# Performance work log

Measured on AMD Instinct MI355X. Metric: run time of the kernel, lower is better.

Reference implementation:

```python
import math
import jax, jax.numpy as jnp
import numpy as np

B, L, D_MODEL = 2, 2048, 768
H = 12            # num_heads == num_key_value_heads
FEAT = 16         # feature_dim
HEAD_DIM = D_MODEL // H  # 64


def taylor_exp(x):
    """Taylor-exp feature map: phi(x) = [1, x/rrd, (x (x) x)/(sqrt(2)*rd)].
    x: [..., d] -> [..., 1 + d + d^2]"""
    d = x.shape[-1]
    rd = math.sqrt(d)
    rrd = math.sqrt(rd)
    r2 = math.sqrt(2.0)
    x2 = (x[..., :, None] * x[..., None, :]).reshape(*x.shape[:-1], d * d) / r2
    ones = jnp.ones(x.shape[:-1] + (1,), dtype=x.dtype)
    return jnp.concatenate([ones, x / rrd, x2 / rd], axis=-1)


def setup_inputs() -> dict:
    key = jax.random.key(0)
    k1, k2, k3, k4, k5 = jax.random.split(key, 5)
    s = 0.02
    return {
        "hidden_states": jax.random.normal(k1, (B, L, D_MODEL), jnp.float32),
        "Wq": jax.random.normal(k2, (H * FEAT, D_MODEL), jnp.float32) * s,
        "Wk": jax.random.normal(k3, (H * FEAT, D_MODEL), jnp.float32) * s,
        "Wv": jax.random.normal(k4, (D_MODEL, D_MODEL), jnp.float32) * s,
        "Wo": jax.random.normal(k5, (D_MODEL, D_MODEL), jnp.float32) * s,
    }


def reference(hidden_states, Wq, Wk, Wv, Wo):
    b, l, d = hidden_states.shape
    # projections (torch Linear, no bias): y = x @ W.T
    q = jnp.einsum('bld,fd->blf', hidden_states, Wq).reshape(b, l, H, FEAT).transpose(0, 2, 1, 3)
    k = jnp.einsum('bld,fd->blf', hidden_states, Wk).reshape(b, l, H, FEAT).transpose(0, 2, 1, 3)
    v = jnp.einsum('bld,fd->blf', hidden_states, Wv).reshape(b, l, H, HEAD_DIM).transpose(0, 2, 1, 3)

    q = taylor_exp(q)   # [b,h,l,Dexp]
    k = taylor_exp(k)   # k_enc == k (forward clones k), v_enc == v

    # denominator: k_enc.sum over seq + causal cumsum of k
    k_state = jnp.sum(k, axis=2, keepdims=True) + jnp.cumsum(k, axis=2)  # [b,h,l,Dexp]
    z = 1.0 / jnp.sum(q * k_state, axis=-1)                              # [b,h,l]

    # quadratic scores; y1 uses causal (tril) mask, y2 uses full scores with same k,v
    A = jnp.einsum('bhnd,bhmd->bhnm', q, k)                              # [b,h,l,l]
    causal = jnp.tril(jnp.ones((l, l), dtype=A.dtype))
    A_total = A * causal + A                                             # tril(A) + A
    y = jnp.einsum('bhnm,bhme->bhne', A_total, v) * z[..., None]         # [b,h,l,e]

    out = y.transpose(0, 2, 1, 3).reshape(b, l, H * HEAD_DIM)
    return jnp.einsum('blf,df->bld', out, Wo)
```

## Files before the change

### kernel.cpp

```cpp
#include <hip/hip_runtime.h>

typedef unsigned short ushortT;
typedef __bf16 bf16x8 __attribute__((ext_vector_type(8)));
typedef float f32x4 __attribute__((ext_vector_type(4)));

#define BB   2
#define LL   2048
#define DM   768
#define HH   12
#define FT   16
#define HD   64
#define DEXP 273
#define CH   128
#define NC   16
#define NBH  24
#define NBLK 384
#define C2f  0.17677669529663687f
#define KH   768
#define KP   1536
#define SLAB_US   4096
#define SPK_BLK_US 36864
#define SPK_BLK_B  73728

__device__ __forceinline__ void split_bf16(float x, ushortT& hi, ushortT& lo) {
  unsigned b = __float_as_uint(x);
  unsigned r = b + 0x7FFFu + ((b >> 16) & 1u);
  hi = (ushortT)(r >> 16);
  float hf = __uint_as_float((unsigned)hi << 16);
  lo = (ushortT)(__float_as_uint(x - hf) >> 16);
}

__global__ __launch_bounds__(256) void pack_a(const float* __restrict__ X,
                                              ushortT* __restrict__ Xh,
                                              int total4) {
  int g = blockIdx.x * 256 + threadIdx.x;
  if (g >= total4) return;
  int m = g / 192, k4 = (g % 192) * 4;
  float4 v = *(const float4*)(X + (size_t)m * 768 + k4);
  ushortT h[4], l[4];
  split_bf16(v.x, h[0], l[0]);
  split_bf16(v.y, h[1], l[1]);
  split_bf16(v.z, h[2], l[2]);
  split_bf16(v.w, h[3], l[3]);
  ushortT* p = Xh + (size_t)m * KP + k4;
  *(ushort4*)p = *(ushort4*)h;
  *(ushort4*)(p + KH) = *(ushort4*)l;
}

__global__ __launch_bounds__(256) void pack_w(const float* __restrict__ W0,
                                              const float* __restrict__ W1,
                                              const float* __restrict__ W2,
                                              int n1, int n2,
                                              ushortT* __restrict__ Wh,
                                              int total4) {
  int g = blockIdx.x * 256 + threadIdx.x;
  if (g >= total4) return;
  int n = g / 192, k4 = (g % 192) * 4;
  const float* src = (n < n1 ? W0 + (size_t)n * 768
                    : n < n2 ? W1 + (size_t)(n - n1) * 768
                             : W2 + (size_t)(n - n2) * 768);
  float4 v = *(const float4*)(src + k4);
  ushortT h[4], l[4];
  split_bf16(v.x, h[0], l[0]);
  split_bf16(v.y, h[1], l[1]);
  split_bf16(v.z, h[2], l[2]);
  split_bf16(v.w, h[3], l[3]);
  ushortT* p = Wh + (size_t)n * KP + k4;
  *(ushort4*)p = *(ushort4*)h;
  *(ushort4*)(p + KH) = *(ushort4*)l;
}

typedef const __attribute__((address_space(1))) unsigned gq_t;
typedef __attribute__((address_space(3))) unsigned lq_t;
__device__ __forceinline__ void gload_lds16(const ushortT* g, ushortT* l) {
  __builtin_amdgcn_global_load_lds((gq_t*)g, (lq_t*)l, 16, 0, 0);
}

__global__ __launch_bounds__(512, 4) void mfma_gemm(const ushortT* __restrict__ A,
                                                    const ushortT* __restrict__ B,
                                                    float* __restrict__ Y, int ldy,
                                                    int ntiles) {
  __shared__ ushortT sAh[2][128 * 32], sAl[2][128 * 32];
  __shared__ ushortT sBh[2][64 * 32], sBl[2][64 * 32];
  const int blk = blockIdx.x;
  const int xcd = blk & 7, slot = blk >> 3;
  const int mtp = gridDim.x / (8 * ntiles);
  const int mt = xcd * mtp + slot / ntiles;
  const int nt = slot % ntiles;
  const int bm = mt * 128, bn = nt * 64;
  const int tid = threadIdx.x, wave = tid >> 6, lane = tid & 63;
  const int srow = lane >> 2, schk = (lane & 3) * 8;
  const ushortT* gsrc;
  ushortT* lb0;
  ushortT* lb1;
  int iters;
  switch (wave) {
    case 0:  gsrc = A + (size_t)(bm + srow) * KP + schk;           lb0 = sAh[0];        lb1 = sAh[1];        iters = 4; break;
    case 1:  gsrc = A + (size_t)(bm + 64 + srow) * KP + schk;      lb0 = sAh[0] + 2048; lb1 = sAh[1] + 2048; iters = 4; break;
    case 2:  gsrc = A + (size_t)(bm + srow) * KP + KH + schk;      lb0 = sAl[0];        lb1 = sAl[1];        iters = 4; break;
    case 3:  gsrc = A + (size_t)(bm + 64 + srow) * KP + KH + schk; lb0 = sAl[0] + 2048; lb1 = sAl[1] + 2048; iters = 4; break;
    case 4:  gsrc = B + (size_t)(bn + srow) * KP + schk;           lb0 = sBh[0];        lb1 = sBh[1];        iters = 2; break;
    case 5:  gsrc = B + (size_t)(bn + 32 + srow) * KP + schk;      lb0 = sBh[0] + 1024; lb1 = sBh[1] + 1024; iters = 2; break;
    case 6:  gsrc = B + (size_t)(bn + srow) * KP + KH + schk;      lb0 = sBl[0];        lb1 = sBl[1];        iters = 2; break;
    default: gsrc = B + (size_t)(bn + 32 + srow) * KP + KH + schk; lb0 = sBl[0] + 1024; lb1 = sBl[1] + 1024; iters = 2; break;
  }
  const int wm = (wave >> 1) * 32, wn = (wave & 1) * 32;
  const int fr = lane & 15, quad = lane >> 4;
  f32x4 acc[2][2] = {};
  for (int it = 0; it < iters; it++)
    gload_lds16(gsrc + (size_t)it * 16 * KP, lb0 + it * 512);
  __syncthreads();
#pragma unroll 2
  for (int step = 0; step < 24; step++) {
    const int cur = step & 1;
    if (step < 23) {
      ushortT* lbn = cur ? lb0 : lb1;
      const int k1 = (step + 1) * 32;
      for (int it = 0; it < iters; it++)
        gload_lds16(gsrc + k1 + (size_t)it * 16 * KP, lbn + it * 512);
    }
    const ushortT* pAh = sAh[cur];
    const ushortT* pAl = sAl[cur];
    const ushortT* pBh = sBh[cur];
    const ushortT* pBl = sBl[cur];
    bf16x8 ah[2], al[2], bh2[2], bl2[2];
#pragma unroll
    for (int mi = 0; mi < 2; mi++) {
      ah[mi] = *(const bf16x8*)&pAh[(wm + mi * 16 + fr) * 32 + quad * 8];
      al[mi] = *(const bf16x8*)&pAl[(wm + mi * 16 + fr) * 32 + quad * 8];
    }
#pragma unroll
    for (int ni = 0; ni < 2; ni++) {
      bh2[ni] = *(const bf16x8*)&pBh[(wn + ni * 16 + fr) * 32 + quad * 8];
      bl2[ni] = *(const bf16x8*)&pBl[(wn + ni * 16 + fr) * 32 + quad * 8];
    }
#pragma unroll
    for (int mi = 0; mi < 2; mi++)
#pragma unroll
      for (int ni = 0; ni < 2; ni++) {
        acc[mi][ni] = __builtin_amdgcn_mfma_f32_16x16x32_bf16(ah[mi], bh2[ni], acc[mi][ni], 0, 0, 0);
        acc[mi][ni] = __builtin_amdgcn_mfma_f32_16x16x32_bf16(ah[mi], bl2[ni], acc[mi][ni], 0, 0, 0);
        acc[mi][ni] = __builtin_amdgcn_mfma_f32_16x16x32_bf16(al[mi], bh2[ni], acc[mi][ni], 0, 0, 0);
      }
    __syncthreads();
  }
  const int orow = quad * 4;
#pragma unroll
  for (int mi = 0; mi < 2; mi++)
#pragma unroll
    for (int ni = 0; ni < 2; ni++) {
      float* yp = Y + (size_t)(bm + wm + mi * 16 + orow) * ldy + bn + wn + ni * 16 + fr;
#pragma unroll
      for (int r = 0; r < 4; r++) yp[(size_t)r * ldy] = acc[mi][ni][r];
    }
}

__global__ __launch_bounds__(512, 4) void chunk_sum_kernel(
    const float* __restrict__ qkv, ushortT* __restrict__ Spk,
    float* __restrict__ csk) {
  const int blk = blockIdx.x;
  const int bh = blk >> 4, c = blk & 15;
  const int b = bh / HH, h = bh % HH;
  __shared__ float kT[16][128];
  __shared__ ushortT phiA[288][72];
  __shared__ ushortT Vt[64][72];
  const float* base = qkv + (size_t)(b * LL + c * CH) * 1152;
  const int tid = threadIdx.x;
  const int wave = tid >> 6, lane = tid & 63;
  const int fr = lane & 15, quad = lane >> 4;
  {
    const int m = tid >> 2, i4 = (tid & 3) * 4;
    float4 k4 = *(const float4*)&base[(size_t)m * 1152 + 192 + h * 16 + i4];
    kT[i4 + 0][m] = k4.x; kT[i4 + 1][m] = k4.y;
    kT[i4 + 2][m] = k4.z; kT[i4 + 3][m] = k4.w;
  }
  const int wm2 = (wave & 1) * 144;
  const int wn2 = (wave >> 1) * 16;
  f32x4 acc[9] = {};
  __syncthreads();
#pragma unroll 1
  for (int s = 0; s < 4; s++) {
    const int m0 = s * 32;
    if (s) __syncthreads();
    {
      const int m = m0 + (tid >> 4), e4 = (tid & 15) * 4;
      float4 v4 = *(const float4*)&base[(size_t)m * 1152 + 384 + h * 64 + e4];
      ushortT hh[4], ll[4];
      split_bf16(v4.x, hh[0], ll[0]); split_bf16(v4.y, hh[1], ll[1]);
      split_bf16(v4.z, hh[2], ll[2]); split_bf16(v4.w, hh[3], ll[3]);
      const int mi2 = m - m0;
#pragma unroll
      for (int j = 0; j < 4; j++) {
        Vt[e4 + j][mi2] = hh[j];
        Vt[e4 + j][32 + mi2] = ll[j];
      }
    }
    for (int idx = tid; idx < 576; idx += 512) {
      const int f = idx >> 1, hf = (idx & 1) * 16;
      const float* pa = (f >= 17) ? kT[(f - 17) >> 4] : (f >= 1 ? kT[f - 1] : kT[0]);
      const float* pb = (f >= 17) ? kT[(f - 17) & 15] : kT[0];
      const float sc = (f == 0) ? 1.0f : (f < 17 ? 0.5f : C2f);
      const bool quadf = (f >= 17);
      const bool valid = (f < DEXP);
      ushortT hrow[16], lrow[16];
#pragma unroll
      for (int g = 0; g < 4; g++) {
        float4 a4 = *(const float4*)&pa[m0 + hf + g * 4];
        float4 b4 = *(const float4*)&pb[m0 + hf + g * 4];
        float v0, v1, v2, v3;
        if (f == 0) {
          v0 = v1 = v2 = v3 = 1.0f;
        } else if (!quadf) {
          v0 = sc * a4.x; v1 = sc * a4.y; v2 = sc * a4.z; v3 = sc * a4.w;
        } else {
          v0 = sc * a4.x * b4.x; v1 = sc * a4.y * b4.y;
          v2 = sc * a4.z * b4.z; v3 = sc * a4.w * b4.w;
        }
        if (!valid) { v0 = v1 = v2 = v3 = 0.0f; }
        split_bf16(v0, hrow[g * 4 + 0], lrow[g * 4 + 0]);
        split_bf16(v1, hrow[g * 4 + 1], lrow[g * 4 + 1]);
        split_bf16(v2, hrow[g * 4 + 2], lrow[g * 4 + 2]);
        split_bf16(v3, hrow[g * 4 + 3], lrow[g * 4 + 3]);
      }
      *(uint4*)&phiA[f][hf] = *(uint4*)&hrow[0];
      *(uint4*)&phiA[f][hf + 8] = *(uint4*)&hrow[8];
      *(uint4*)&phiA[f][32 + hf] = *(uint4*)&lrow[0];
      *(uint4*)&phiA[f][32 + hf + 8] = *(uint4*)&lrow[8];
    }
    __syncthreads();
    bf16x8 bhf = *(const bf16x8*)&Vt[wn2 + fr][quad * 8];
    bf16x8 blf = *(const bf16x8*)&Vt[wn2 + fr][32 + quad * 8];
#pragma unroll
    for (int mi = 0; mi < 9; mi++) {
      bf16x8 ah = *(const bf16x8*)&phiA[wm2 + mi * 16 + fr][quad * 8];
      bf16x8 al = *(const bf16x8*)&phiA[wm2 + mi * 16 + fr][32 + quad * 8];
      acc[mi] = __builtin_amdgcn_mfma_f32_16x16x32_bf16(ah, bhf, acc[mi], 0, 0, 0);
      acc[mi] = __builtin_amdgcn_mfma_f32_16x16x32_bf16(ah, blf, acc[mi], 0, 0, 0);
      acc[mi] = __builtin_amdgcn_mfma_f32_16x16x32_bf16(al, bhf, acc[mi], 0, 0, 0);
    }
  }
  for (int f = tid; f < DEXP; f += 512) {
    float sum = 0.0f;
    if (f == 0) {
      sum = (float)CH;
    } else if (f < 17) {
      const float* p = kT[f - 1];
      for (int m = 0; m < CH; m += 4) {
        float4 x = *(const float4*)&p[m];
        sum += x.x + x.y + x.z + x.w;
      }
      sum *= 0.5f;
    } else {
      const float* pa2 = kT[(f - 17) >> 4];
      const float* pb2 = kT[(f - 17) & 15];
      for (int m = 0; m < CH; m += 4) {
        float4 x = *(const float4*)&pa2[m];
        float4 y = *(const float4*)&pb2[m];
        sum += x.x * y.x + x.y * y.y + x.z * y.z + x.w * y.w;
      }
      sum *= C2f;
    }
    csk[(size_t)blk * DEXP + f] = sum;
  }
  __syncthreads();
  ushortT* stage = &phiA[0][0];
  ushortT* Sp = Spk + (size_t)blk * SPK_BLK_US;
#pragma unroll 1
  for (int sl = 0; sl < 9; sl++) {
    if (sl) __syncthreads();
#pragma unroll
    for (int mi = 0; mi < 9; mi++) {
      const int fb = wm2 + mi * 16;
      if ((fb >> 5) == sl) {
        const int fi0 = (fb & 31) + quad * 4;
        const int gh = fi0 >> 3;
        const int inner = (fi0 << 1) & 15;
        const int e = wn2 + fr;
        const int es = (e & 7) << 4;
        ushortT hh2[4], ll2[4];
#pragma unroll
        for (int r = 0; r < 4; r++) split_bf16(acc[mi][r], hh2[r], ll2[r]);
        char* rowp = (char*)stage + e * 128;
        *(ushort4*)(rowp + ((gh << 4) ^ es) + inner) = *(ushort4*)hh2;
        *(ushort4*)(rowp + (((gh + 4) << 4) ^ es) + inner) = *(ushort4*)ll2;
      }
    }
    __syncthreads();
    uint4* gdst = (uint4*)(Sp + (size_t)sl * SLAB_US);
    const uint4* lsrc = (const uint4*)stage;
    gdst[tid] = lsrc[tid];
  }
}

__global__ __launch_bounds__(256) void prefix_kernel(ushortT* __restrict__ Spk,
                                                     float* __restrict__ csk) {
  const int gid = blockIdx.x * 256 + threadIdx.x;
  const int totS = NBH * 4608;
  if (gid < totS) {
    const int bh = gid / 4608;
    const int rem = gid % 4608;
    const int slab = rem >> 9;
    const int e = (rem >> 3) & 63;
    const int wp = rem & 7;
    const int es = (e & 7) << 4;
    const unsigned off_h = e * 128 + ((((wp >> 1)) << 4) ^ es) + ((wp & 1) << 3);
    const unsigned off_l = e * 128 + ((((wp >> 1) + 4) << 4) ^ es) + ((wp & 1) << 3);
    char* base = (char*)Spk + (size_t)bh * NC * SPK_BLK_B + slab * 8192;
    float r0[NC], r1[NC], r2[NC], r3[NC];
    float t0 = 0.f, t1 = 0.f, t2 = 0.f, t3 = 0.f;
#pragma unroll
    for (int cc = 0; cc < NC; cc++) {
      const char* p = base + (size_t)cc * SPK_BLK_B;
      ushort4 hw = *(const ushort4*)(p + off_h);
      ushort4 lw = *(const ushort4*)(p + off_l);
      r0[cc] = __uint_as_float((unsigned)hw.x << 16) + __uint_as_float((unsigned)lw.x << 16);
      r1[cc] = __uint_as_float((unsigned)hw.y << 16) + __uint_as_float((unsigned)lw.y << 16);
      r2[cc] = __uint_as_float((unsigned)hw.z << 16) + __uint_as_float((unsigned)lw.z << 16);
      r3[cc] = __uint_as_float((unsigned)hw.w << 16) + __uint_as_float((unsigned)lw.w << 16);
      t0 += r0[cc]; t1 += r1[cc]; t2 += r2[cc]; t3 += r3[cc];
    }
    float u0 = 0.f, u1 = 0.f, u2 = 0.f, u3 = 0.f;
#pragma unroll
    for (int cc = 0; cc < NC; cc++) {
      ushort4 hw, lw;
      split_bf16(u0 + t0, hw.x, lw.x);
      split_bf16(u1 + t1, hw.y, lw.y);
      split_bf16(u2 + t2, hw.z, lw.z);
      split_bf16(u3 + t3, hw.w, lw.w);
      char* p = base + (size_t)cc * SPK_BLK_B;
      *(ushort4*)(p + off_h) = hw;
      *(ushort4*)(p + off_l) = lw;
      u0 += r0[cc]; u1 += r1[cc]; u2 += r2[cc]; u3 += r3[cc];
    }
  } else {
    const int g2 = gid - totS;
    if (g2 < NBH * DEXP) {
      const int bh = g2 / DEXP;
      const int f = g2 % DEXP;
      float r[NC];
      float tot = 0.0f;
#pragma unroll
      for (int cc = 0; cc < NC; cc++) {
        r[cc] = csk[(size_t)(bh * NC + cc) * DEXP + f];
        tot += r[cc];
      }
      float run = 0.0f;
#pragma unroll
      for (int cc = 0; cc < NC; cc++) {
        csk[(size_t)(bh * NC + cc) * DEXP + f] = run + tot;
        run += r[cc];
      }
    }
  }
}

__global__ __launch_bounds__(512, 4) void fused_out(
    const float* __restrict__ qkv, const ushortT* __restrict__ Spk,
    const float* __restrict__ csk, ushortT* __restrict__ Ahat) {
  const int blk = blockIdx.x;
  const int bh = blk >> 4, c = blk & 15;
  const int b = bh / HH, h = bh % HH;
  __shared__ ushortT phiA[128][72];
  __shared__ ushortT GtD[2][4096];
  __shared__ ushortT qA1[128][24];
  __shared__ ushortT qA2[128][24];
  __shared__ ushortT kB[32][40];
  __shared__ ushortT gkS[9][64];
  __shared__ ushortT zero64[64];
  __shared__ ushortT onesRow[64];
  __shared__ float zl[128];
  const int tid = threadIdx.x;
  const int wv = tid >> 6, lane = tid & 63;
  const int fr = lane & 15, quad = lane >> 4;
  const int prow = tid >> 2, pq = tid & 3;
  const float* base = qkv + (size_t)(b * LL + c * CH) * 1152;
  const float* qrow = base + (size_t)prow * 1152 + h * 16;
  const ushortT* Gp = Spk + (size_t)blk * SPK_BLK_US;
  float qr[16];
#pragma unroll
  for (int i = 0; i < 4; i++) {
    float4 v = *(const float4*)(qrow + i * 4);
    qr[i * 4 + 0] = v.x; qr[i * 4 + 1] = v.y;
    qr[i * 4 + 2] = v.z; qr[i * 4 + 3] = v.w;
  }
  gload_lds16(Gp + wv * 512 + lane * 8, &GtD[0][wv * 512]);
  {
    ushortT qh4[4], ql4[4];
#pragma unroll
    for (int i = 0; i < 4; i++) split_bf16(qr[pq * 4 + i], qh4[i], ql4[i]);
    *(ushort4*)&qA1[prow][pq * 4] = *(ushort4*)qh4;
    *(ushort4*)&qA2[prow][pq * 4] = *(ushort4*)ql4;
  }
  {
    const float* gkp = csk + (size_t)blk * DEXP;
    for (int f = tid; f < 288; f += 512) {
      float v = (f < DEXP) ? gkp[f] : 0.0f;
      ushortT hh, ll;
      split_bf16(v, hh, ll);
      gkS[f >> 5][f & 31] = hh;
      gkS[f >> 5][32 + (f & 31)] = ll;
    }
  }
  if (tid < 64) {
    zero64[tid] = 0;
    onesRow[tid] = (tid < 32) ? (ushortT)0x3F80 : (ushortT)0;
  }
  f32x4 acc[5] = {};
#pragma unroll 1
  for (int s = 0; s < 9; s++) {
    __syncthreads();
    if (s < 8)
      gload_lds16(Gp + (s + 1) * SLAB_US + wv * 512 + lane * 8,
                  &GtD[(s + 1) & 1][wv * 512]);
    const int f0 = s * 32;
    {
      ushortT h8[8], l8[8];
#pragma unroll
      for (int j = 0; j < 8; j++) {
        const int f = f0 + pq * 8 + j;
        float v;
        if (f == 0) v = 1.0f;
        else if (f < 17) v = 0.5f * qr[f - 1];
        else if (f < DEXP) {
          const int ii = f - 17;
          v = C2f * qr[ii >> 4] * qr[ii & 15];
        } else v = 0.0f;
        split_bf16(v, h8[j], l8[j]);
      }
      *(uint4*)&phiA[prow][pq * 8] = *(uint4*)&h8[0];
      *(uint4*)&phiA[prow][32 + pq * 8] = *(uint4*)&l8[0];
    }
    bf16x8 ah = *(const bf16x8*)&phiA[wv * 16 + fr][quad * 8];
    bf16x8 al = *(const bf16x8*)&phiA[wv * 16 + fr][32 + quad * 8];
    const char* gt = (const char*)&GtD[s & 1][0];
    const int sw = (fr & 7) << 4;
#pragma unroll
    for (int ni = 0; ni < 4; ni++) {
      const int rb = (ni * 16 + fr) * 128;
      bf16x8 bh2 = *(const bf16x8*)(gt + rb + ((quad * 16) ^ sw));
      bf16x8 bl2 = *(const bf16x8*)(gt + rb + ((64 + quad * 16) ^ sw));
      acc[ni] = __builtin_amdgcn_mfma_f32_16x16x32_bf16(ah, bh2, acc[ni], 0, 0, 0);
      acc[ni] = __builtin_amdgcn_mfma_f32_16x16x32_bf16(ah, bl2, acc[ni], 0, 0, 0);
      acc[ni] = __builtin_amdgcn_mfma_f32_16x16x32_bf16(al, bh2, acc[ni], 0, 0, 0);
    }
    {
      const ushortT* gp = (fr == 0) ? &gkS[s][0] : &zero64[0];
      bf16x8 gh = *(const bf16x8*)(gp + quad * 8);
      bf16x8 gl = *(const bf16x8*)(gp + 32 + quad * 8);
      acc[4] = __builtin_amdgcn_mfma_f32_16x16x32_bf16(ah, gh, acc[4], 0, 0, 0);
      acc[4] = __builtin_amdgcn_mfma_f32_16x16x32_bf16(ah, gl, acc[4], 0, 0, 0);
      acc[4] = __builtin_amdgcn_mfma_f32_16x16x32_bf16(al, gh, acc[4], 0, 0, 0);
    }
  }
  __syncthreads();
  ushortT* VtF = &GtD[0][0];
#pragma unroll 1
  for (int s = 0; s < 4; s++) {
    const int m0 = s * 32;
    if (tid < 128) {
      int mL = tid >> 2, i4 = (tid & 3) * 4;
      float4 k4 = *(const float4*)&base[(size_t)(m0 + mL) * 1152 + 192 + h * 16 + i4];
      ushortT hh[4], ll[4];
      split_bf16(k4.x, hh[0], ll[0]); split_bf16(k4.y, hh[1], ll[1]);
      split_bf16(k4.z, hh[2], ll[2]); split_bf16(k4.w, hh[3], ll[3]);
      *(ushort4*)&kB[mL][i4] = *(ushort4*)hh;
      *(ushort4*)&kB[mL][16 + i4] = *(ushort4*)ll;
    }
    {
      int mL = tid >> 4, e4 = (tid & 15) * 4;
      float4 v4 = *(const float4*)&base[(size_t)(m0 + mL) * 1152 + 384 + h * 64 + e4];
      ushortT hh[4], ll[4];
      split_bf16(v4.x, hh[0], ll[0]); split_bf16(v4.y, hh[1], ll[1]);
      split_bf16(v4.z, hh[2], ll[2]); split_bf16(v4.w, hh[3], ll[3]);
#pragma unroll
      for (int j = 0; j < 4; j++) {
        VtF[(e4 + j) * 72 + mL] = hh[j];
        VtF[(e4 + j) * 72 + 32 + mL] = ll[j];
      }
    }
    __syncthreads();
    if (s <= (wv >> 1)) {
      bf16x8 a1 = *(const bf16x8*)&qA1[wv * 16 + fr][(quad & 1) * 8];
      bf16x8 a2 = *(const bf16x8*)&qA2[wv * 16 + fr][(quad & 1) * 8];
#pragma unroll
      for (int mtt = 0; mtt < 2; mtt++) {
        bf16x8 bk = *(const bf16x8*)&kB[mtt * 16 + fr][quad * 8];
        f32x4 sf = {};
        sf = __builtin_amdgcn_mfma_f32_16x16x32_bf16(a1, bk, sf, 0, 0, 0);
        sf = __builtin_amdgcn_mfma_f32_16x16x32_bf16(a2, bk, sf, 0, 0, 0);
        const int mg = m0 + mtt * 16 + fr;
#pragma unroll
        for (int r = 0; r < 4; r++) {
          const int rowL = wv * 16 + quad * 4 + r;
          const float sv = sf[r];
          const float p = (mg <= rowL) ? fmaf(sv, fmaf(sv, 0.03125f, 0.25f), 1.0f) : 0.0f;
          ushortT ph, pl;
          split_bf16(p, ph, pl);
          phiA[rowL][mtt * 16 + fr] = ph;
          phiA[rowL][32 + mtt * 16 + fr] = pl;
        }
      }
      bf16x8 ah = *(const bf16x8*)&phiA[wv * 16 + fr][quad * 8];
      bf16x8 al = *(const bf16x8*)&phiA[wv * 16 + fr][32 + quad * 8];
#pragma unroll
      for (int ni = 0; ni < 4; ni++) {
        bf16x8 bh2 = *(const bf16x8*)&VtF[(ni * 16 + fr) * 72 + quad * 8];
        bf16x8 bl2 = *(const bf16x8*)&VtF[(ni * 16 + fr) * 72 + 32 + quad * 8];
        acc[ni] = __builtin_amdgcn_mfma_f32_16x16x32_bf16(ah, bh2, acc[ni], 0, 0, 0);
        acc[ni] = __builtin_amdgcn_mfma_f32_16x16x32_bf16(ah, bl2, acc[ni], 0, 0, 0);
        acc[ni] = __builtin_amdgcn_mfma_f32_16x16x32_bf16(al, bh2, acc[ni], 0, 0, 0);
      }
      {
        const ushortT* op = (fr == 0) ? &onesRow[0] : &zero64[0];
        bf16x8 oh = *(const bf16x8*)(op + quad * 8);
        acc[4] = __builtin_amdgcn_mfma_f32_16x16x32_bf16(ah, oh, acc[4], 0, 0, 0);
        acc[4] = __builtin_amdgcn_mfma_f32_16x16x32_bf16(al, oh, acc[4], 0, 0, 0);
      }
    }
    __syncthreads();
  }
  if (fr == 0) {
#pragma unroll
    for (int r = 0; r < 4; r++) {
      const int rowL = wv * 16 + quad * 4 + r;
      zl[rowL] = 1.0f / acc[4][r];
    }
  }
  const size_t rowbase = (size_t)(b * LL + c * CH);
#pragma unroll
  for (int ni = 0; ni < 4; ni++)
#pragma unroll
    for (int r = 0; r < 4; r++) {
      const int rowL = wv * 16 + quad * 4 + r;
      const float val = acc[ni][r] * zl[rowL];
      ushortT hh, ll;
      split_bf16(val, hh, ll);
      ushortT* ap = Ahat + (rowbase + rowL) * (size_t)KP + h * 64 + ni * 16 + fr;
      ap[0] = hh;
      ap[KH] = ll;
    }
}

extern "C" void kernel_launch(void* const* d_in, const int* in_sizes, int n_in,
                              void* d_out, int out_size, void* d_ws, size_t ws_size,
                              hipStream_t stream) {
  const float* hs = (const float*)d_in[0];
  const float* Wq = (const float*)d_in[1];
  const float* Wk = (const float*)d_in[2];
  const float* Wv = (const float*)d_in[3];
  const float* Wo = (const float*)d_in[4];
  float* out = (float*)d_out;
  char* ws = (char*)d_ws;
  float* qkv = (float*)(ws);
  char*  attR = ws + 18874368;
  ushortT* Spk = (ushortT*)(ws + 31457280);
  float* csk = (float*)(ws + 59768832);
  ushortT* Xhat = (ushortT*)(ws + 31457280);
  ushortT* What = (ushortT*)attR;
  ushortT* Ahat = (ushortT*)attR;
  ushortT* Wohat = (ushortT*)qkv;
  const dim3 thr(256);
  pack_a<<<3072, thr, 0, stream>>>(hs, Xhat, 4096 * 192);
  pack_w<<<864, thr, 0, stream>>>(Wq, Wk, Wv, 192, 384, What, 1152 * 192);
  mfma_gemm<<<576, dim3(512), 0, stream>>>(Xhat, What, qkv, 1152, 18);
  chunk_sum_kernel<<<NBLK, dim3(512), 0, stream>>>(qkv, Spk, csk);
  {
    const int tot = NBH * 4608 + NBH * DEXP;
    prefix_kernel<<<(tot + 255) / 256, thr, 0, stream>>>(Spk, csk);
  }
  fused_out<<<NBLK, dim3(512), 0, stream>>>(qkv, Spk, csk, Ahat);
  pack_w<<<576, thr, 0, stream>>>(Wo, Wo, Wo, 768, 768, Wohat, 768 * 192);
  mfma_gemm<<<384, dim3(512), 0, stream>>>(Ahat, Wohat, out, DM, 12);
}
```

Baseline: 227.9 us.

## Triple-buffer LDS prefetch with explicit vmcnt waits in GEMM and fused_out

Both the split-bf16 MFMA GEMM and the fused_out slab loop move from double to triple LDS buffering. Each stage now has two loads in flight. A per-wave s_waitcnt vmcnt plus a raw s_barrier replaces the full __syncthreads at each step, and the trailing barrier after the MFMAs is removed. The goal is to hide global-to-LDS load latency behind MFMA work and to cut barrier stalls. The cost is more LDS per block, which may lower occupancy, and hand-counted vmcnt waits that are fragile if the load counts change.

```diff
diff --git a/kernel.cpp b/kernel.cpp
--- a/kernel.cpp
+++ b/kernel.cpp
@@ -80,8 +80,8 @@
                                                     const ushortT* __restrict__ B,
                                                     float* __restrict__ Y, int ldy,
                                                     int ntiles) {
-  __shared__ ushortT sAh[2][128 * 32], sAl[2][128 * 32];
-  __shared__ ushortT sBh[2][64 * 32], sBl[2][64 * 32];
+  __shared__ ushortT sAh[3 * 4096], sAl[3 * 4096];
+  __shared__ ushortT sBh[3 * 2048], sBl[3 * 2048];
   const int blk = blockIdx.x;
   const int xcd = blk & 7, slot = blk >> 3;
   const int mtp = gridDim.x / (8 * ntiles);
@@ -91,38 +91,47 @@
   const int tid = threadIdx.x, wave = tid >> 6, lane = tid & 63;
   const int srow = lane >> 2, schk = (lane & 3) * 8;
   const ushortT* gsrc;
-  ushortT* lb0;
-  ushortT* lb1;
-  int iters;
+  ushortT* dstbase;
+  int bufstride, dstoff, iters;
   switch (wave) {
-    case 0:  gsrc = A + (size_t)(bm + srow) * KP + schk;           lb0 = sAh[0];        lb1 = sAh[1];        iters = 4; break;
-    case 1:  gsrc = A + (size_t)(bm + 64 + srow) * KP + schk;      lb0 = sAh[0] + 2048; lb1 = sAh[1] + 2048; iters = 4; break;
-    case 2:  gsrc = A + (size_t)(bm + srow) * KP + KH + schk;      lb0 = sAl[0];        lb1 = sAl[1];        iters = 4; break;
-    case 3:  gsrc = A + (size_t)(bm + 64 + srow) * KP + KH + schk; lb0 = sAl[0] + 2048; lb1 = sAl[1] + 2048; iters = 4; break;
-    case 4:  gsrc = B + (size_t)(bn + srow) * KP + schk;           lb0 = sBh[0];        lb1 = sBh[1];        iters = 2; break;
-    case 5:  gsrc = B + (size_t)(bn + 32 + srow) * KP + schk;      lb0 = sBh[0] + 1024; lb1 = sBh[1] + 1024; iters = 2; break;
-    case 6:  gsrc = B + (size_t)(bn + srow) * KP + KH + schk;      lb0 = sBl[0];        lb1 = sBl[1];        iters = 2; break;
-    default: gsrc = B + (size_t)(bn + 32 + srow) * KP + KH + schk; lb0 = sBl[0] + 1024; lb1 = sBl[1] + 1024; iters = 2; break;
+    case 0:  gsrc = A + (size_t)(bm + srow) * KP + schk;           dstbase = sAh; bufstride = 4096; dstoff = 0;    iters = 4; break;
+    case 1:  gsrc = A + (size_t)(bm + 64 + srow) * KP + schk;      dstbase = sAh; bufstride = 4096; dstoff = 2048; iters = 4; break;
+    case 2:  gsrc = A + (size_t)(bm + srow) * KP + KH + schk;      dstbase = sAl; bufstride = 4096; dstoff = 0;    iters = 4; break;
+    case 3:  gsrc = A + (size_t)(bm + 64 + srow) * KP + KH + schk; dstbase = sAl; bufstride = 4096; dstoff = 2048; iters = 4; break;
+    case 4:  gsrc = B + (size_t)(bn + srow) * KP + schk;           dstbase = sBh; bufstride = 2048; dstoff = 0;    iters = 2; break;
+    case 5:  gsrc = B + (size_t)(bn + 32 + srow) * KP + schk;      dstbase = sBh; bufstride = 2048; dstoff = 1024; iters = 2; break;
+    case 6:  gsrc = B + (size_t)(bn + srow) * KP + KH + schk;      dstbase = sBl; bufstride = 2048; dstoff = 0;    iters = 2; break;
+    default: gsrc = B + (size_t)(bn + 32 + srow) * KP + KH + schk; dstbase = sBl; bufstride = 2048; dstoff = 1024; iters = 2; break;
   }
   const int wm = (wave >> 1) * 32, wn = (wave & 1) * 32;
   const int fr = lane & 15, quad = lane >> 4;
   f32x4 acc[2][2] = {};
   for (int it = 0; it < iters; it++)
-    gload_lds16(gsrc + (size_t)it * 16 * KP, lb0 + it * 512);
-  __syncthreads();
-#pragma unroll 2
+    gload_lds16(gsrc + (size_t)it * 16 * KP, dstbase + dstoff + it * 512);
+  for (int it = 0; it < iters; it++)
+    gload_lds16(gsrc + 32 + (size_t)it * 16 * KP, dstbase + bufstride + dstoff + it * 512);
+#pragma unroll 1
   for (int step = 0; step < 24; step++) {
-    const int cur = step & 1;
     if (step < 23) {
-      ushortT* lbn = cur ? lb0 : lb1;
-      const int k1 = (step + 1) * 32;
+      if (wave < 4) { asm volatile("s_waitcnt vmcnt(4)" ::: "memory"); }
+      else          { asm volatile("s_waitcnt vmcnt(2)" ::: "memory"); }
+    } else {
+      asm volatile("s_waitcnt vmcnt(0)" ::: "memory");
+    }
+    __builtin_amdgcn_sched_barrier(0);
+    __builtin_amdgcn_s_barrier();
+    __builtin_amdgcn_sched_barrier(0);
+    if (step < 22) {
+      ushortT* lbn = dstbase + ((step + 2) % 3) * bufstride + dstoff;
+      const int k1 = (step + 2) * 32;
       for (int it = 0; it < iters; it++)
         gload_lds16(gsrc + k1 + (size_t)it * 16 * KP, lbn + it * 512);
     }
-    const ushortT* pAh = sAh[cur];
-    const ushortT* pAl = sAl[cur];
-    const ushortT* pBh = sBh[cur];
-    const ushortT* pBl = sBl[cur];
+    const int cur = step % 3;
+    const ushortT* pAh = sAh + cur * 4096;
+    const ushortT* pAl = sAl + cur * 4096;
+    const ushortT* pBh = sBh + cur * 2048;
+    const ushortT* pBl = sBl + cur * 2048;
     bf16x8 ah[2], al[2], bh2[2], bl2[2];
 #pragma unroll
     for (int mi = 0; mi < 2; mi++) {
@@ -142,7 +151,6 @@
         acc[mi][ni] = __builtin_amdgcn_mfma_f32_16x16x32_bf16(ah[mi], bl2[ni], acc[mi][ni], 0, 0, 0);
         acc[mi][ni] = __builtin_amdgcn_mfma_f32_16x16x32_bf16(al[mi], bh2[ni], acc[mi][ni], 0, 0, 0);
       }
-    __syncthreads();
   }
   const int orow = quad * 4;
 #pragma unroll
@@ -361,7 +369,7 @@
   const int bh = blk >> 4, c = blk & 15;
   const int b = bh / HH, h = bh % HH;
   __shared__ ushortT phiA[128][72];
-  __shared__ ushortT GtD[2][4096];
+  __shared__ ushortT GtD3[3 * 4096];
   __shared__ ushortT qA1[128][24];
   __shared__ ushortT qA2[128][24];
   __shared__ ushortT kB[32][40];
@@ -383,7 +391,8 @@
     qr[i * 4 + 0] = v.x; qr[i * 4 + 1] = v.y;
     qr[i * 4 + 2] = v.z; qr[i * 4 + 3] = v.w;
   }
-  gload_lds16(Gp + wv * 512 + lane * 8, &GtD[0][wv * 512]);
+  gload_lds16(Gp + wv * 512 + lane * 8, GtD3 + wv * 512);
+  gload_lds16(Gp + SLAB_US + wv * 512 + lane * 8, GtD3 + 4096 + wv * 512);
   {
     ushortT qh4[4], ql4[4];
 #pragma unroll
@@ -406,12 +415,17 @@
     onesRow[tid] = (tid < 32) ? (ushortT)0x3F80 : (ushortT)0;
   }
   f32x4 acc[5] = {};
+  asm volatile("s_waitcnt lgkmcnt(0)" ::: "memory");
 #pragma unroll 1
   for (int s = 0; s < 9; s++) {
-    __syncthreads();
-    if (s < 8)
-      gload_lds16(Gp + (s + 1) * SLAB_US + wv * 512 + lane * 8,
-                  &GtD[(s + 1) & 1][wv * 512]);
+    if (s < 8) { asm volatile("s_waitcnt vmcnt(1)" ::: "memory"); }
+    else       { asm volatile("s_waitcnt vmcnt(0)" ::: "memory"); }
+    __builtin_amdgcn_sched_barrier(0);
+    __builtin_amdgcn_s_barrier();
+    __builtin_amdgcn_sched_barrier(0);
+    if (s < 7)
+      gload_lds16(Gp + (s + 2) * SLAB_US + wv * 512 + lane * 8,
+                  GtD3 + ((s + 2) % 3) * 4096 + wv * 512);
     const int f0 = s * 32;
     {
       ushortT h8[8], l8[8];
@@ -432,7 +446,7 @@
     }
     bf16x8 ah = *(const bf16x8*)&phiA[wv * 16 + fr][quad * 8];
     bf16x8 al = *(const bf16x8*)&phiA[wv * 16 + fr][32 + quad * 8];
-    const char* gt = (const char*)&GtD[s & 1][0];
+    const char* gt = (const char*)(GtD3 + (s % 3) * 4096);
     const int sw = (fr & 7) << 4;
 #pragma unroll
     for (int ni = 0; ni < 4; ni++) {
@@ -453,7 +467,7 @@
     }
   }
   __syncthreads();
-  ushortT* VtF = &GtD[0][0];
+  ushortT* VtF = &GtD3[0];
 #pragma unroll 1
   for (int s = 0; s < 4; s++) {
     const int m0 = s * 32;
```

Result: no change. 231.5 us (+1.6%).
